# Kernel optimization log

Hardware: AMD Instinct MI355X
Metric: run time of the kernel (lower is better)

## Reference

```python
import jax, jax.numpy as jnp
import numpy as np


def setup_inputs() -> dict:
    key = jax.random.key(0)
    ks = jax.random.split(key, 6)
    B, H, W, C = 2, 96, 96, 64
    x = jax.random.normal(ks[0], (B, H, W, C), dtype=jnp.float32)
    # 1x1 conv weights as [C_in, C_out] matrices (kernel size 1)
    W1 = jax.random.normal(ks[1], (C, C // 8), dtype=jnp.float32) * 0.1
    b1 = jnp.zeros((C // 8,), dtype=jnp.float32)
    W2 = jax.random.normal(ks[2], (C, C // 8), dtype=jnp.float32) * 0.1
    b2 = jnp.zeros((C // 8,), dtype=jnp.float32)
    W3 = jax.random.normal(ks[3], (C, C // 2), dtype=jnp.float32) * 0.1
    b3 = jnp.zeros((C // 2,), dtype=jnp.float32)
    W4 = jax.random.normal(ks[4], (C // 2, C), dtype=jnp.float32) * 0.1
    b4 = jnp.zeros((C,), dtype=jnp.float32)
    gamma = jax.random.uniform(ks[5], (1,), dtype=jnp.float32)
    return {"x": x, "W1": W1, "b1": b1, "W2": W2, "b2": b2,
            "W3": W3, "b3": b3, "W4": W4, "b4": b4, "gamma": gamma}


def reference(x, W1, b1, W2, b2, W3, b3, W4, b4, gamma):
    B, H, W_, C = x.shape
    N = H * W_
    # 1x1 convs == per-pixel matmuls
    f = jnp.einsum('bhwc,cd->bhwd', x, W1) + b1   # [B,H,W,C/8] (key)
    g = jnp.einsum('bhwc,cd->bhwd', x, W2) + b2   # [B,H,W,C/8] (query)
    h = jnp.einsum('bhwc,cd->bhwd', x, W3) + b3   # [B,H,W,C/2] (value)
    f = f.reshape(B, N, -1)
    g = g.reshape(B, N, -1)
    h = h.reshape(B, N, -1)
    s = jnp.einsum('bnd,bmd->bnm', g, f)          # [B,N,N] full score matrix
    beta = jax.nn.softmax(s, axis=-1)
    o = jnp.einsum('bnm,bmd->bnd', beta, h)       # [B,N,C/2]
    o = o.reshape(B, H, W_, C // 2)
    o = jnp.einsum('bhwc,cd->bhwd', o, W4) + b4   # [B,H,W,C]
    return gamma[0] * o + x
```

## Files before the change

kernel.cpp:

```cpp
#include <hip/hip_runtime.h>
#include <hip/hip_bf16.h>


#define BATCH 2
#define NTOK 9216
#define CCH 64
#define DV 32
#define KS 8
#define KEYS_PER_BLOCK (NTOK / KS)
#define KEYS_PER_WAVE (KEYS_PER_BLOCK / 2)
#define KT 32
#define NKT (KEYS_PER_WAVE / KT)
#define ROWS (BATCH * NTOK)
#define QT (ROWS / 32)
#define NKTILE (NTOK / 32)
#define LOG2E 1.44269504088896340736f
#define PB 32
#define ZTOT 152064

typedef __attribute__((ext_vector_type(8))) short bf16x8;
typedef __attribute__((ext_vector_type(4))) float f32x4;

__device__ __forceinline__ short f2bf(float x) {
    __hip_bfloat16 h = __float2bfloat16(x);
    return *(short*)&h;
}
__device__ __forceinline__ float bf2f(short s) {
    unsigned u = ((unsigned)(unsigned short)s) << 16;
    return *(float*)&u;
}

__global__ __launch_bounds__(512) void proj_kernel(
    const float* __restrict__ x,
    const float* __restrict__ W1, const float* __restrict__ b1,
    const float* __restrict__ W2, const float* __restrict__ b2,
    const float* __restrict__ W3, const float* __restrict__ b3,
    short* __restrict__ fx, short* __restrict__ gx, short* __restrict__ hTi,
    float4* __restrict__ zbase)
{
    __shared__ float xS[PB][CCH];
    __shared__ short fgS[2][PB][32];
    __shared__ short hS[32][PB + 2];

    const int tid = threadIdx.x;
    const int r0  = blockIdx.x * PB;

    {
        int zi = blockIdx.x * 512 + tid;
        if (zi < ZTOT) zbase[zi] = make_float4(0.f, 0.f, 0.f, 0.f);
    }

    ((float4*)xS)[tid] = ((const float4*)(x + (size_t)r0 * CCH))[tid];
    __syncthreads();

    {
        const int half = tid >> 8;
        const int rr   = (tid & 255) >> 3;
        const int c    = tid & 7;
        const float* xr = xS[rr];
        if (half == 0) {
            float acc = b1[c];
            #pragma unroll
            for (int k = 0; k < CCH; ++k) acc += xr[k] * W1[k * 8 + c];
            short hi = f2bf(acc);
            short lo = f2bf(acc - bf2f(hi));
            fgS[0][rr][c] = hi; fgS[0][rr][c + 8] = hi;
            fgS[0][rr][c + 16] = lo; fgS[0][rr][c + 24] = 0;
        } else {
            float acc = b2[c];
            #pragma unroll
            for (int k = 0; k < CCH; ++k) acc += xr[k] * W2[k * 8 + c];
            acc *= LOG2E;
            short hi = f2bf(acc);
            short lo = f2bf(acc - bf2f(hi));
            fgS[1][rr][c] = hi; fgS[1][rr][c + 8] = lo;
            fgS[1][rr][c + 16] = hi; fgS[1][rr][c + 24] = 0;
        }
    }
    {
        const int c = tid & 31;
        const int rbase = tid >> 5;
        #pragma unroll
        for (int s = 0; s < 2; ++s) {
            int rr = rbase + s * 16;
            float acc = b3[c];
            #pragma unroll
            for (int k = 0; k < CCH; ++k) acc += xS[rr][k] * W3[k * 32 + c];
            int np = ((rr & 15) >> 2) * 8 + (rr & 3) + ((rr >> 4) & 1) * 4;
            hS[c][np] = f2bf(acc);
        }
    }
    __syncthreads();

    ((int*)(fx + (size_t)r0 * 32))[tid] = ((const int*)fgS[0])[tid];
    ((int*)(gx + (size_t)r0 * 32))[tid] = ((const int*)fgS[1])[tid];
    {
        const int b  = r0 / NTOK;
        const int n0 = r0 - b * NTOK;
        const int kt = n0 >> 5;
        const int c  = tid >> 4;
        const int d  = tid & 15;
        ((int*)(hTi + ((size_t)(b * NKTILE + kt)) * 1024))[c * 16 + d] =
            ((const int*)&hS[c][0])[d];
    }
}

__global__ __launch_bounds__(128, 4) void attn_kernel(
    const short* __restrict__ fx, const short* __restrict__ gx,
    const short* __restrict__ hTi,
    float* __restrict__ l_acc, float* __restrict__ o_acc)
{
    __shared__ float red[32 * 33];

    const int tid  = threadIdx.x;
    const int wave = tid >> 6;
    const int lane = tid & 63;
    const int col  = lane & 15;
    const int quad = lane >> 4;

    const int blk = blockIdx.x;
    const int qt  = blk % QT;
    const int ks  = blk / QT;
    const int b   = qt / (QT / BATCH);
    const int qbase   = (qt % (QT / BATCH)) * 32;
    const int rowbase = b * NTOK + qbase;

    const bf16x8 agA = *(const bf16x8*)(gx + (size_t)(rowbase + col) * 32 + quad * 8);
    const bf16x8 agB = *(const bf16x8*)(gx + (size_t)(rowbase + 16 + col) * 32 + quad * 8);

    f32x4 oA0 = {0.f,0.f,0.f,0.f}, oA1 = {0.f,0.f,0.f,0.f};
    f32x4 oB0 = {0.f,0.f,0.f,0.f}, oB1 = {0.f,0.f,0.f,0.f};
    float lA = 0.f, lB = 0.f;
    const f32x4 zero4 = {0.f,0.f,0.f,0.f};

    const int kstart = ks * KEYS_PER_BLOCK + wave * KEYS_PER_WAVE;
    const short* fbase = fx + ((size_t)b * NTOK + kstart) * 32;
    const short* hbase = hTi + ((size_t)(b * NKTILE) + (kstart >> 5)) * 1024
                             + col * 32 + quad * 8;

    bf16x8 fa0 = *(const bf16x8*)(fbase + (size_t)col * 32 + quad * 8);
    bf16x8 fa1 = *(const bf16x8*)(fbase + (size_t)(16 + col) * 32 + quad * 8);
    bf16x8 hb0 = *(const bf16x8*)(hbase);
    bf16x8 hb1 = *(const bf16x8*)(hbase + 512);

    union PU { int i[4]; bf16x8 v; };

    for (int t = 0; t < NKT; ++t) {
        f32x4 t00 = __builtin_amdgcn_mfma_f32_16x16x32_bf16(fa0, agA, zero4, 0, 0, 0);
        f32x4 t01 = __builtin_amdgcn_mfma_f32_16x16x32_bf16(fa1, agA, zero4, 0, 0, 0);
        f32x4 t10 = __builtin_amdgcn_mfma_f32_16x16x32_bf16(fa0, agB, zero4, 0, 0, 0);
        f32x4 t11 = __builtin_amdgcn_mfma_f32_16x16x32_bf16(fa1, agB, zero4, 0, 0, 0);

        const int kn = (t + 1 < NKT) ? (t + 1) : 0;
        bf16x8 nf0 = *(const bf16x8*)(fbase + (size_t)(kn * KT + col) * 32 + quad * 8);
        bf16x8 nf1 = *(const bf16x8*)(fbase + (size_t)(kn * KT + 16 + col) * 32 + quad * 8);
        bf16x8 nh0 = *(const bf16x8*)(hbase + kn * 1024);
        bf16x8 nh1 = *(const bf16x8*)(hbase + kn * 1024 + 512);

        PU pA, pB;
        {
            float e0 = __builtin_amdgcn_exp2f(t00[0]), e1 = __builtin_amdgcn_exp2f(t00[1]);
            float e2 = __builtin_amdgcn_exp2f(t00[2]), e3 = __builtin_amdgcn_exp2f(t00[3]);
            float e4 = __builtin_amdgcn_exp2f(t01[0]), e5 = __builtin_amdgcn_exp2f(t01[1]);
            float e6 = __builtin_amdgcn_exp2f(t01[2]), e7 = __builtin_amdgcn_exp2f(t01[3]);
            lA += (e0 + e1) + (e2 + e3) + (e4 + e5) + (e6 + e7);
            pA.i[0] = (int)__builtin_amdgcn_perm((unsigned)__float_as_int(e1) + 0x8000u,
                                                 (unsigned)__float_as_int(e0) + 0x8000u, 0x07060302u);
            pA.i[1] = (int)__builtin_amdgcn_perm((unsigned)__float_as_int(e3) + 0x8000u,
                                                 (unsigned)__float_as_int(e2) + 0x8000u, 0x07060302u);
            pA.i[2] = (int)__builtin_amdgcn_perm((unsigned)__float_as_int(e5) + 0x8000u,
                                                 (unsigned)__float_as_int(e4) + 0x8000u, 0x07060302u);
            pA.i[3] = (int)__builtin_amdgcn_perm((unsigned)__float_as_int(e7) + 0x8000u,
                                                 (unsigned)__float_as_int(e6) + 0x8000u, 0x07060302u);
        }
        {
            float e0 = __builtin_amdgcn_exp2f(t10[0]), e1 = __builtin_amdgcn_exp2f(t10[1]);
            float e2 = __builtin_amdgcn_exp2f(t10[2]), e3 = __builtin_amdgcn_exp2f(t10[3]);
            float e4 = __builtin_amdgcn_exp2f(t11[0]), e5 = __builtin_amdgcn_exp2f(t11[1]);
            float e6 = __builtin_amdgcn_exp2f(t11[2]), e7 = __builtin_amdgcn_exp2f(t11[3]);
            lB += (e0 + e1) + (e2 + e3) + (e4 + e5) + (e6 + e7);
            pB.i[0] = (int)__builtin_amdgcn_perm((unsigned)__float_as_int(e1) + 0x8000u,
                                                 (unsigned)__float_as_int(e0) + 0x8000u, 0x07060302u);
            pB.i[1] = (int)__builtin_amdgcn_perm((unsigned)__float_as_int(e3) + 0x8000u,
                                                 (unsigned)__float_as_int(e2) + 0x8000u, 0x07060302u);
            pB.i[2] = (int)__builtin_amdgcn_perm((unsigned)__float_as_int(e5) + 0x8000u,
                                                 (unsigned)__float_as_int(e4) + 0x8000u, 0x07060302u);
            pB.i[3] = (int)__builtin_amdgcn_perm((unsigned)__float_as_int(e7) + 0x8000u,
                                                 (unsigned)__float_as_int(e6) + 0x8000u, 0x07060302u);
        }

        oA0 = __builtin_amdgcn_mfma_f32_16x16x32_bf16(pA.v, hb0, oA0, 0, 0, 0);
        oA1 = __builtin_amdgcn_mfma_f32_16x16x32_bf16(pA.v, hb1, oA1, 0, 0, 0);
        oB0 = __builtin_amdgcn_mfma_f32_16x16x32_bf16(pB.v, hb0, oB0, 0, 0, 0);
        oB1 = __builtin_amdgcn_mfma_f32_16x16x32_bf16(pB.v, hb1, oB1, 0, 0, 0);

        fa0 = nf0; fa1 = nf1; hb0 = nh0; hb1 = nh1;
    }

    lA += __shfl_xor(lA, 16); lA += __shfl_xor(lA, 32);
    lB += __shfl_xor(lB, 16); lB += __shfl_xor(lB, 32);

    if (wave == 1) {
        #pragma unroll
        for (int r = 0; r < 4; ++r) {
            red[(quad * 4 + r) * 33 + col]           = oA0[r];
            red[(quad * 4 + r) * 33 + 16 + col]      = oA1[r];
            red[(16 + quad * 4 + r) * 33 + col]      = oB0[r];
            red[(16 + quad * 4 + r) * 33 + 16 + col] = oB1[r];
        }
        if (quad == 0) {
            red[col * 33 + 32]        = lA;
            red[(16 + col) * 33 + 32] = lB;
        }
    }
    __syncthreads();
    if (wave == 0) {
        #pragma unroll
        for (int r = 0; r < 4; ++r) {
            int qA = quad * 4 + r, qB = 16 + quad * 4 + r;
            atomicAdd(&o_acc[(size_t)(rowbase + qA) * 32 + col],      oA0[r] + red[qA * 33 + col]);
            atomicAdd(&o_acc[(size_t)(rowbase + qA) * 32 + 16 + col], oA1[r] + red[qA * 33 + 16 + col]);
            atomicAdd(&o_acc[(size_t)(rowbase + qB) * 32 + col],      oB0[r] + red[qB * 33 + col]);
            atomicAdd(&o_acc[(size_t)(rowbase + qB) * 32 + 16 + col], oB1[r] + red[qB * 33 + 16 + col]);
        }
        if (quad == 0) {
            atomicAdd(&l_acc[rowbase + col],      lA + red[col * 33 + 32]);
            atomicAdd(&l_acc[rowbase + 16 + col], lB + red[(16 + col) * 33 + 32]);
        }
    }
}

__global__ __launch_bounds__(256) void merge_kernel(
    const float* __restrict__ l_acc, const float* __restrict__ o_acc,
    const float* __restrict__ x,
    const float* __restrict__ W4, const float* __restrict__ b4,
    const float* __restrict__ gamma, float* __restrict__ out)
{
    __shared__ float oS[4][DV];
    int wave = threadIdx.x >> 6;
    int lane = threadIdx.x & 63;
    int row  = blockIdx.x * 4 + wave;

    float invL = 1.f / l_acc[row];
    if (lane < DV) {
        oS[wave][lane] = o_acc[(size_t)row * DV + lane] * invL;
    }
    __syncthreads();

    float dot = b4[lane];
    #pragma unroll
    for (int k = 0; k < DV; ++k) dot += oS[wave][k] * W4[k * 64 + lane];
    float gm  = gamma[0];
    float res = x[(size_t)row * 64 + lane];
    out[(size_t)row * 64 + lane] = gm * dot + res;
}

extern "C" void kernel_launch(void* const* d_in, const int* in_sizes, int n_in,
                              void* d_out, int out_size, void* d_ws, size_t ws_size,
                              hipStream_t stream) {
    const float* x     = (const float*)d_in[0];
    const float* W1    = (const float*)d_in[1];
    const float* b1    = (const float*)d_in[2];
    const float* W2    = (const float*)d_in[3];
    const float* b2    = (const float*)d_in[4];
    const float* W3    = (const float*)d_in[5];
    const float* b3    = (const float*)d_in[6];
    const float* W4    = (const float*)d_in[7];
    const float* b4    = (const float*)d_in[8];
    const float* gamma = (const float*)d_in[9];
    float* out = (float*)d_out;

    short* fx    = (short*)d_ws;
    short* gx    = fx + (size_t)ROWS * 32;
    short* hTi   = gx + (size_t)ROWS * 32;
    float* l_acc = (float*)(hTi + (size_t)ROWS * 32);
    float* o_acc = l_acc + ROWS;

    proj_kernel<<<ROWS / PB, 512, 0, stream>>>(
        x, W1, b1, W2, b2, W3, b3, fx, gx, hTi, (float4*)l_acc);

    attn_kernel<<<QT * KS, 128, 0, stream>>>(fx, gx, hTi, l_acc, o_acc);

    merge_kernel<<<ROWS / 4, 256, 0, stream>>>(l_acc, o_acc, x, W4, b4, gamma, out);
}
```

Measured before the change: 140.3 us.

## Process 64 query rows per attention block to reuse key/value loads

Doubles the query tile per attention block from 32 to 64 rows, so each loaded key and value fragment feeds four query sub-tiles instead of two. This halves the block count and the global traffic for keys and values per query. The cost is more accumulator registers per thread, which may lower occupancy under the launch bound of 4, and fewer blocks to fill the GPU.

```diff
diff --git a/kernel.cpp b/kernel.cpp
--- a/kernel.cpp
+++ b/kernel.cpp
@@ -12,7 +12,7 @@
 #define KT 32
 #define NKT (KEYS_PER_WAVE / KT)
 #define ROWS (BATCH * NTOK)
-#define QT (ROWS / 32)
+#define QTB (ROWS / 64)
 #define NKTILE (NTOK / 32)
 #define LOG2E 1.44269504088896340736f
 #define PB 32
@@ -110,7 +110,7 @@
     const short* __restrict__ hTi,
     float* __restrict__ l_acc, float* __restrict__ o_acc)
 {
-    __shared__ float red[32 * 33];
+    __shared__ float red[64 * 33];
 
     const int tid  = threadIdx.x;
     const int wave = tid >> 6;
@@ -119,19 +119,23 @@
     const int quad = lane >> 4;
 
     const int blk = blockIdx.x;
-    const int qt  = blk % QT;
-    const int ks  = blk / QT;
-    const int b   = qt / (QT / BATCH);
-    const int qbase   = (qt % (QT / BATCH)) * 32;
+    const int qt  = blk % QTB;
+    const int ks  = blk / QTB;
+    const int b   = qt / (QTB / BATCH);
+    const int qbase   = (qt % (QTB / BATCH)) * 64;
     const int rowbase = b * NTOK + qbase;
 
     const bf16x8 agA = *(const bf16x8*)(gx + (size_t)(rowbase + col) * 32 + quad * 8);
     const bf16x8 agB = *(const bf16x8*)(gx + (size_t)(rowbase + 16 + col) * 32 + quad * 8);
-
-    f32x4 oA0 = {0.f,0.f,0.f,0.f}, oA1 = {0.f,0.f,0.f,0.f};
-    f32x4 oB0 = {0.f,0.f,0.f,0.f}, oB1 = {0.f,0.f,0.f,0.f};
-    float lA = 0.f, lB = 0.f;
-    const f32x4 zero4 = {0.f,0.f,0.f,0.f};
+    const bf16x8 agC = *(const bf16x8*)(gx + (size_t)(rowbase + 32 + col) * 32 + quad * 8);
+    const bf16x8 agD = *(const bf16x8*)(gx + (size_t)(rowbase + 48 + col) * 32 + quad * 8);
+
+    f32x4 oA0 = {0,0,0,0}, oA1 = {0,0,0,0};
+    f32x4 oB0 = {0,0,0,0}, oB1 = {0,0,0,0};
+    f32x4 oC0 = {0,0,0,0}, oC1 = {0,0,0,0};
+    f32x4 oD0 = {0,0,0,0}, oD1 = {0,0,0,0};
+    float lA = 0.f, lB = 0.f, lC = 0.f, lD = 0.f;
+    const f32x4 zero4 = {0,0,0,0};
 
     const int kstart = ks * KEYS_PER_BLOCK + wave * KEYS_PER_WAVE;
     const short* fbase = fx + ((size_t)b * NTOK + kstart) * 32;
@@ -145,11 +149,32 @@
 
     union PU { int i[4]; bf16x8 v; };
 
+    #define EXPPACK(T0, T1, LSUM, P)                                            \
+    {                                                                           \
+        float e0 = __builtin_amdgcn_exp2f(T0[0]), e1 = __builtin_amdgcn_exp2f(T0[1]); \
+        float e2 = __builtin_amdgcn_exp2f(T0[2]), e3 = __builtin_amdgcn_exp2f(T0[3]); \
+        float e4 = __builtin_amdgcn_exp2f(T1[0]), e5 = __builtin_amdgcn_exp2f(T1[1]); \
+        float e6 = __builtin_amdgcn_exp2f(T1[2]), e7 = __builtin_amdgcn_exp2f(T1[3]); \
+        LSUM += (e0 + e1) + (e2 + e3) + (e4 + e5) + (e6 + e7);                  \
+        P.i[0] = (int)__builtin_amdgcn_perm((unsigned)__float_as_int(e1) + 0x8000u, \
+                                            (unsigned)__float_as_int(e0) + 0x8000u, 0x07060302u); \
+        P.i[1] = (int)__builtin_amdgcn_perm((unsigned)__float_as_int(e3) + 0x8000u, \
+                                            (unsigned)__float_as_int(e2) + 0x8000u, 0x07060302u); \
+        P.i[2] = (int)__builtin_amdgcn_perm((unsigned)__float_as_int(e5) + 0x8000u, \
+                                            (unsigned)__float_as_int(e4) + 0x8000u, 0x07060302u); \
+        P.i[3] = (int)__builtin_amdgcn_perm((unsigned)__float_as_int(e7) + 0x8000u, \
+                                            (unsigned)__float_as_int(e6) + 0x8000u, 0x07060302u); \
+    }
+
     for (int t = 0; t < NKT; ++t) {
-        f32x4 t00 = __builtin_amdgcn_mfma_f32_16x16x32_bf16(fa0, agA, zero4, 0, 0, 0);
-        f32x4 t01 = __builtin_amdgcn_mfma_f32_16x16x32_bf16(fa1, agA, zero4, 0, 0, 0);
-        f32x4 t10 = __builtin_amdgcn_mfma_f32_16x16x32_bf16(fa0, agB, zero4, 0, 0, 0);
-        f32x4 t11 = __builtin_amdgcn_mfma_f32_16x16x32_bf16(fa1, agB, zero4, 0, 0, 0);
+        f32x4 tA0 = __builtin_amdgcn_mfma_f32_16x16x32_bf16(fa0, agA, zero4, 0, 0, 0);
+        f32x4 tA1 = __builtin_amdgcn_mfma_f32_16x16x32_bf16(fa1, agA, zero4, 0, 0, 0);
+        f32x4 tB0 = __builtin_amdgcn_mfma_f32_16x16x32_bf16(fa0, agB, zero4, 0, 0, 0);
+        f32x4 tB1 = __builtin_amdgcn_mfma_f32_16x16x32_bf16(fa1, agB, zero4, 0, 0, 0);
+        f32x4 tC0 = __builtin_amdgcn_mfma_f32_16x16x32_bf16(fa0, agC, zero4, 0, 0, 0);
+        f32x4 tC1 = __builtin_amdgcn_mfma_f32_16x16x32_bf16(fa1, agC, zero4, 0, 0, 0);
+        f32x4 tD0 = __builtin_amdgcn_mfma_f32_16x16x32_bf16(fa0, agD, zero4, 0, 0, 0);
+        f32x4 tD1 = __builtin_amdgcn_mfma_f32_16x16x32_bf16(fa1, agD, zero4, 0, 0, 0);
 
         const int kn = (t + 1 < NKT) ? (t + 1) : 0;
         bf16x8 nf0 = *(const bf16x8*)(fbase + (size_t)(kn * KT + col) * 32 + quad * 8);
@@ -157,75 +182,68 @@
         bf16x8 nh0 = *(const bf16x8*)(hbase + kn * 1024);
         bf16x8 nh1 = *(const bf16x8*)(hbase + kn * 1024 + 512);
 
-        PU pA, pB;
-        {
-            float e0 = __builtin_amdgcn_exp2f(t00[0]), e1 = __builtin_amdgcn_exp2f(t00[1]);
-            float e2 = __builtin_amdgcn_exp2f(t00[2]), e3 = __builtin_amdgcn_exp2f(t00[3]);
-            float e4 = __builtin_amdgcn_exp2f(t01[0]), e5 = __builtin_amdgcn_exp2f(t01[1]);
-            float e6 = __builtin_amdgcn_exp2f(t01[2]), e7 = __builtin_amdgcn_exp2f(t01[3]);
-            lA += (e0 + e1) + (e2 + e3) + (e4 + e5) + (e6 + e7);
-            pA.i[0] = (int)__builtin_amdgcn_perm((unsigned)__float_as_int(e1) + 0x8000u,
-                                                 (unsigned)__float_as_int(e0) + 0x8000u, 0x07060302u);
-            pA.i[1] = (int)__builtin_amdgcn_perm((unsigned)__float_as_int(e3) + 0x8000u,
-                                                 (unsigned)__float_as_int(e2) + 0x8000u, 0x07060302u);
-            pA.i[2] = (int)__builtin_amdgcn_perm((unsigned)__float_as_int(e5) + 0x8000u,
-                                                 (unsigned)__float_as_int(e4) + 0x8000u, 0x07060302u);
-            pA.i[3] = (int)__builtin_amdgcn_perm((unsigned)__float_as_int(e7) + 0x8000u,
-                                                 (unsigned)__float_as_int(e6) + 0x8000u, 0x07060302u);
-        }
-        {
-            float e0 = __builtin_amdgcn_exp2f(t10[0]), e1 = __builtin_amdgcn_exp2f(t10[1]);
-            float e2 = __builtin_amdgcn_exp2f(t10[2]), e3 = __builtin_amdgcn_exp2f(t10[3]);
-            float e4 = __builtin_amdgcn_exp2f(t11[0]), e5 = __builtin_amdgcn_exp2f(t11[1]);
-            float e6 = __builtin_amdgcn_exp2f(t11[2]), e7 = __builtin_amdgcn_exp2f(t11[3]);
-            lB += (e0 + e1) + (e2 + e3) + (e4 + e5) + (e6 + e7);
-            pB.i[0] = (int)__builtin_amdgcn_perm((unsigned)__float_as_int(e1) + 0x8000u,
-                                                 (unsigned)__float_as_int(e0) + 0x8000u, 0x07060302u);
-            pB.i[1] = (int)__builtin_amdgcn_perm((unsigned)__float_as_int(e3) + 0x8000u,
-                                                 (unsigned)__float_as_int(e2) + 0x8000u, 0x07060302u);
-            pB.i[2] = (int)__builtin_amdgcn_perm((unsigned)__float_as_int(e5) + 0x8000u,
-                                                 (unsigned)__float_as_int(e4) + 0x8000u, 0x07060302u);
-            pB.i[3] = (int)__builtin_amdgcn_perm((unsigned)__float_as_int(e7) + 0x8000u,
-                                                 (unsigned)__float_as_int(e6) + 0x8000u, 0x07060302u);
-        }
-
+        PU pA, pB, pC, pD;
+        EXPPACK(tA0, tA1, lA, pA)
+        EXPPACK(tB0, tB1, lB, pB)
         oA0 = __builtin_amdgcn_mfma_f32_16x16x32_bf16(pA.v, hb0, oA0, 0, 0, 0);
         oA1 = __builtin_amdgcn_mfma_f32_16x16x32_bf16(pA.v, hb1, oA1, 0, 0, 0);
         oB0 = __builtin_amdgcn_mfma_f32_16x16x32_bf16(pB.v, hb0, oB0, 0, 0, 0);
         oB1 = __builtin_amdgcn_mfma_f32_16x16x32_bf16(pB.v, hb1, oB1, 0, 0, 0);
+        EXPPACK(tC0, tC1, lC, pC)
+        EXPPACK(tD0, tD1, lD, pD)
+        oC0 = __builtin_amdgcn_mfma_f32_16x16x32_bf16(pC.v, hb0, oC0, 0, 0, 0);
+        oC1 = __builtin_amdgcn_mfma_f32_16x16x32_bf16(pC.v, hb1, oC1, 0, 0, 0);
+        oD0 = __builtin_amdgcn_mfma_f32_16x16x32_bf16(pD.v, hb0, oD0, 0, 0, 0);
+        oD1 = __builtin_amdgcn_mfma_f32_16x16x32_bf16(pD.v, hb1, oD1, 0, 0, 0);
 
         fa0 = nf0; fa1 = nf1; hb0 = nh0; hb1 = nh1;
     }
+    #undef EXPPACK
 
     lA += __shfl_xor(lA, 16); lA += __shfl_xor(lA, 32);
     lB += __shfl_xor(lB, 16); lB += __shfl_xor(lB, 32);
+    lC += __shfl_xor(lC, 16); lC += __shfl_xor(lC, 32);
+    lD += __shfl_xor(lD, 16); lD += __shfl_xor(lD, 32);
 
     if (wave == 1) {
         #pragma unroll
         for (int r = 0; r < 4; ++r) {
-            red[(quad * 4 + r) * 33 + col]           = oA0[r];
-            red[(quad * 4 + r) * 33 + 16 + col]      = oA1[r];
-            red[(16 + quad * 4 + r) * 33 + col]      = oB0[r];
-            red[(16 + quad * 4 + r) * 33 + 16 + col] = oB1[r];
+            int q = quad * 4 + r;
+            red[(q)      * 33 + col]      = oA0[r];
+            red[(q)      * 33 + 16 + col] = oA1[r];
+            red[(q + 16) * 33 + col]      = oB0[r];
+            red[(q + 16) * 33 + 16 + col] = oB1[r];
+            red[(q + 32) * 33 + col]      = oC0[r];
+            red[(q + 32) * 33 + 16 + col] = oC1[r];
+            red[(q + 48) * 33 + col]      = oD0[r];
+            red[(q + 48) * 33 + 16 + col] = oD1[r];
         }
         if (quad == 0) {
-            red[col * 33 + 32]        = lA;
-            red[(16 + col) * 33 + 32] = lB;
+            red[(col)      * 33 + 32] = lA;
+            red[(col + 16) * 33 + 32] = lB;
+            red[(col + 32) * 33 + 32] = lC;
+            red[(col + 48) * 33 + 32] = lD;
         }
     }
     __syncthreads();
     if (wave == 0) {
         #pragma unroll
         for (int r = 0; r < 4; ++r) {
-            int qA = quad * 4 + r, qB = 16 + quad * 4 + r;
-            atomicAdd(&o_acc[(size_t)(rowbase + qA) * 32 + col],      oA0[r] + red[qA * 33 + col]);
-            atomicAdd(&o_acc[(size_t)(rowbase + qA) * 32 + 16 + col], oA1[r] + red[qA * 33 + 16 + col]);
-            atomicAdd(&o_acc[(size_t)(rowbase + qB) * 32 + col],      oB0[r] + red[qB * 33 + col]);
-            atomicAdd(&o_acc[(size_t)(rowbase + qB) * 32 + 16 + col], oB1[r] + red[qB * 33 + 16 + col]);
+            int q = quad * 4 + r;
+            atomicAdd(&o_acc[(size_t)(rowbase + q)      * 32 + col],      oA0[r] + red[(q)      * 33 + col]);
+            atomicAdd(&o_acc[(size_t)(rowbase + q)      * 32 + 16 + col], oA1[r] + red[(q)      * 33 + 16 + col]);
+            atomicAdd(&o_acc[(size_t)(rowbase + q + 16) * 32 + col],      oB0[r] + red[(q + 16) * 33 + col]);
+            atomicAdd(&o_acc[(size_t)(rowbase + q + 16) * 32 + 16 + col], oB1[r] + red[(q + 16) * 33 + 16 + col]);
+            atomicAdd(&o_acc[(size_t)(rowbase + q + 32) * 32 + col],      oC0[r] + red[(q + 32) * 33 + col]);
+            atomicAdd(&o_acc[(size_t)(rowbase + q + 32) * 32 + 16 + col], oC1[r] + red[(q + 32) * 33 + 16 + col]);
+            atomicAdd(&o_acc[(size_t)(rowbase + q + 48) * 32 + col],      oD0[r] + red[(q + 48) * 33 + col]);
+            atomicAdd(&o_acc[(size_t)(rowbase + q + 48) * 32 + 16 + col], oD1[r] + red[(q + 48) * 33 + 16 + col]);
         }
         if (quad == 0) {
-            atomicAdd(&l_acc[rowbase + col],      lA + red[col * 33 + 32]);
-            atomicAdd(&l_acc[rowbase + 16 + col], lB + red[(16 + col) * 33 + 32]);
+            atomicAdd(&l_acc[rowbase + col],      lA + red[(col)      * 33 + 32]);
+            atomicAdd(&l_acc[rowbase + 16 + col], lB + red[(col + 16) * 33 + 32]);
+            atomicAdd(&l_acc[rowbase + 32 + col], lC + red[(col + 32) * 33 + 32]);
+            atomicAdd(&l_acc[rowbase + 48 + col], lD + red[(col + 48) * 33 + 32]);
         }
     }
 }
@@ -279,7 +297,7 @@
     proj_kernel<<<ROWS / PB, 512, 0, stream>>>(
         x, W1, b1, W2, b2, W3, b3, fx, gx, hTi, (float4*)l_acc);
 
-    attn_kernel<<<QT * KS, 128, 0, stream>>>(fx, gx, hTi, l_acc, o_acc);
+    attn_kernel<<<QTB * KS, 128, 0, stream>>>(fx, gx, hTi, l_acc, o_acc);
 
     merge_kernel<<<ROWS / 4, 256, 0, stream>>>(l_acc, o_acc, x, W4, b4, gamma, out);
 }
```

After: 139.2 us. About the same (-0.8%).
